# Optimization experiments

Measured on AMD Instinct MI355X. Metric: run time of the kernel, lower is better.

The kernel has to match this reference:

```python
import jax, jax.numpy as jnp
import numpy as np


def log_g(x):
    # log of g(x) = where(x>=0, x+0.5, sigmoid(x))
    return jnp.where(x >= 0, jnp.log(jax.nn.relu(x) + 0.5), -jax.nn.softplus(-x))


def heinsen_scan_log(log_coeffs, log_values):
    # associative scan in log space over seq dim (axis=1)
    a_star = jnp.cumsum(log_coeffs, axis=1)
    log_h0_plus_b_star = jax.lax.cumlogsumexp(log_values - a_star, axis=1)
    return jnp.exp(a_star + log_h0_plus_b_star)


def setup_inputs() -> dict:
    key = jax.random.key(0)
    k1, k2, k3 = jax.random.split(key, 3)
    B, S, D_IN, D_INNER, D_OUT = 4, 4096, 1024, 1024, 1024
    x = jax.random.normal(k1, (B, S, D_IN), dtype=jnp.float32)
    # xavier_normal for Linear(d_in, 2*d_inner): std = sqrt(2/(fan_in+fan_out))
    std_hg = float(np.sqrt(2.0 / (D_IN + 2 * D_INNER)))
    W_hg = jax.random.normal(k2, (2 * D_INNER, D_IN), dtype=jnp.float32) * std_hg
    std_out = float(np.sqrt(2.0 / (D_INNER + D_OUT)))
    W_out = jax.random.normal(k3, (D_OUT, D_INNER), dtype=jnp.float32) * std_out
    return {"x": x, "W_hg": W_hg, "W_out": W_out}


def reference(x, W_hg, W_out):
    # x: [B,S,Din]; W_hg: [2*Dinner, Din]; W_out: [Dout, Dinner]
    hg = jnp.einsum("bsd,ed->bse", x, W_hg)
    hidden, gate = jnp.split(hg, 2, axis=-1)
    log_coeffs = -jax.nn.softplus(gate)        # log(1 - z)
    log_z = -jax.nn.softplus(-gate)            # log(z)
    log_values = log_z + log_g(hidden)
    h = heinsen_scan_log(log_coeffs, log_values)  # [B,S,Dinner]
    out = jnp.einsum("bsd,od->bso", h, W_out)
    return out
```

## Files before the change

### kernel.cpp

```cpp
#include <hip/hip_runtime.h>
#include <math.h>


typedef unsigned short ushort_t;
typedef unsigned int uint_t;
typedef __attribute__((ext_vector_type(4))) float f32x4;
typedef __attribute__((ext_vector_type(8))) __bf16 bf16x8;
typedef __attribute__((ext_vector_type(8))) unsigned short u16x8;

constexpr int Bsz  = 4;
constexpr int S    = 4096;
constexpr int Din  = 1024;
constexpr int Dh   = 1024;
constexpr int M    = Bsz * S;
constexpr int NCH  = 64;
constexpr int CL   = S / NCH;

__device__ __forceinline__ unsigned short f2bf(float f) {
    unsigned int u = __float_as_uint(f);
    unsigned int r = (u + 0x7fffu + ((u >> 16) & 1u)) >> 16;
    return (unsigned short)r;
}
__device__ __forceinline__ float bf2f(unsigned short u) {
    return __uint_as_float(((unsigned int)u) << 16);
}
__device__ __forceinline__ float sigf(float x) {
    x = fminf(fmaxf(x, -30.f), 30.f);
    return 1.0f / (1.0f + __expf(-x));
}
__device__ __forceinline__ void gld_lds16(const ushort_t* g, ushort_t* l) {
    __builtin_amdgcn_global_load_lds(
        (const __attribute__((address_space(1))) void*)g,
        (__attribute__((address_space(3))) void*)l, 16, 0, 0);
}

__global__ __launch_bounds__(256) void cvt_all(
    const float* __restrict__ x, const float* __restrict__ whg,
    const float* __restrict__ wout,
    ushort_t* __restrict__ xb, ushort_t* __restrict__ whgb,
    ushort_t* __restrict__ woutb)
{
    constexpr int NX = M * Din / 8;
    constexpr int NW = 2048 * 1024 / 8;
    const int i = blockIdx.x * 256 + threadIdx.x;
    const float* src; ushort_t* dst; int k;
    if (i < NX)            { src = x;    dst = xb;    k = i; }
    else if (i < NX + NW)  { src = whg;  dst = whgb;  k = i - NX; }
    else                   { src = wout; dst = woutb; k = i - NX - NW; }
    const float4 a = ((const float4*)src)[(size_t)k * 2];
    const float4 b = ((const float4*)src)[(size_t)k * 2 + 1];
    u16x8 o;
    o[0] = f2bf(a.x); o[1] = f2bf(a.y); o[2] = f2bf(a.z); o[3] = f2bf(a.w);
    o[4] = f2bf(b.x); o[5] = f2bf(b.y); o[6] = f2bf(b.z); o[7] = f2bf(b.w);
    ((u16x8*)dst)[k] = o;
}

__global__ __launch_bounds__(512, 2) void gemm256(
    const ushort_t* __restrict__ A, int lda,
    const ushort_t* __restrict__ B, int ldb,
    ushort_t* __restrict__ Cout, int ldc, int K, int nbx_log2)
{
    __shared__ ushort_t lds[4][2][8192];

    const int P = K >> 5;

    const int nwg = gridDim.x;
    const int cpx = nwg >> 3;
    const int bid = blockIdx.x;
    const int swz = (bid & 7) * cpx + (bid >> 3);
    const int bx  = swz & ((1 << nbx_log2) - 1);
    const int by  = swz >> nbx_log2;
    const int bm0 = by * 256;
    const int bn0 = bx * 256;

    const int t  = threadIdx.x;
    const int w  = t >> 6;
    const int l  = t & 63;
    const int wr = w >> 2;
    const int wc = w & 3;

    const int fr = l & 15;
    const int kg = l >> 4;
    const int qp = kg ^ (((fr >> 3) & 1) << 1);
    const int a_base = wr * 4096 + fr * 32 + qp * 8;
    const int b_base = wc * 2048 + fr * 32 + qp * 8;

    const int rs = l >> 2;
    const int lq = (l & 3) ^ (((rs >> 3) & 1) << 1);
    const ushort_t* gA0 = A + (size_t)(bm0 + w * 16 + rs) * lda + lq * 8;
    const ushort_t* gA1 = gA0 + (size_t)128 * lda;
    const ushort_t* gB0 = B + (size_t)(bn0 + w * 16 + rs) * ldb + lq * 8;
    const ushort_t* gB1 = gB0 + (size_t)128 * ldb;

    f32x4 acc[8][4];
    #pragma unroll
    for (int i = 0; i < 8; ++i)
        #pragma unroll
        for (int j = 0; j < 4; ++j)
            acc[i][j] = (f32x4){0.f, 0.f, 0.f, 0.f};

    auto stage = [&](int p) {
        const int s2 = p & 3;
        const int ko = p * 32;
        gld_lds16(gA0 + ko, &lds[s2][0][w * 512]);
        gld_lds16(gA1 + ko, &lds[s2][0][w * 512 + 4096]);
        gld_lds16(gB0 + ko, &lds[s2][1][w * 512]);
        gld_lds16(gB1 + ko, &lds[s2][1][w * 512 + 4096]);
    };

    auto phase_body = [&](int p, bool do_stage) {
        __builtin_amdgcn_s_barrier();
        __builtin_amdgcn_sched_barrier(0);
        const int s = p & 3;
        const ushort_t* la = &lds[s][0][0];
        const ushort_t* lb = &lds[s][1][0];
        bf16x8 af[8], bfr[4];
        #pragma unroll
        for (int i = 0; i < 8; ++i)
            af[i] = *reinterpret_cast<const bf16x8*>(&la[a_base + i * 512]);
        #pragma unroll
        for (int j = 0; j < 4; ++j)
            bfr[j] = *reinterpret_cast<const bf16x8*>(&lb[b_base + j * 512]);
        if (do_stage) stage(p + 2);
        __builtin_amdgcn_sched_barrier(0);
        __builtin_amdgcn_s_setprio(1);
        #pragma unroll
        for (int i = 0; i < 8; ++i)
            #pragma unroll
            for (int j = 0; j < 4; ++j)
                acc[i][j] = __builtin_amdgcn_mfma_f32_16x16x32_bf16(
                    af[i], bfr[j], acc[i][j], 0, 0, 0);
        __builtin_amdgcn_s_setprio(0);
        __builtin_amdgcn_sched_barrier(0);
    };

    stage(0);
    stage(1);

    for (int p = 0; p < P - 1; ++p) {
        asm volatile("s_waitcnt vmcnt(4)" ::: "memory");
        phase_body(p, p < P - 2);
    }
    asm volatile("s_waitcnt vmcnt(0)" ::: "memory");
    phase_body(P - 1, false);

    #pragma unroll
    for (int i = 0; i < 8; ++i) {
        #pragma unroll
        for (int j = 0; j < 4; ++j) {
            const int col = bn0 + wc * 64 + j * 16 + fr;
            #pragma unroll
            for (int r = 0; r < 4; ++r) {
                const int row = bm0 + wr * 128 + i * 16 + kg * 4 + r;
                Cout[(size_t)row * ldc + col] = f2bf(acc[i][j][r]);
            }
        }
    }
}

__global__ __launch_bounds__(512, 4) void gemm128(
    const ushort_t* __restrict__ A, int lda,
    const ushort_t* __restrict__ B, int ldb,
    float* __restrict__ Cout, int ldc, int K, int nbx_log2)
{
    __shared__ ushort_t lds[3][12288];

    const int P = K >> 5;

    const int nwg = gridDim.x;
    const int cpx = nwg >> 3;
    const int bid = blockIdx.x;
    const int swz = (bid & 7) * cpx + (bid >> 3);
    const int bx  = swz & ((1 << nbx_log2) - 1);
    const int by  = swz >> nbx_log2;
    const int bm0 = by * 128;
    const int bn0 = bx * 256;

    const int t  = threadIdx.x;
    const int w  = t >> 6;
    const int l  = t & 63;
    const int wr = w >> 2;
    const int wc = w & 3;

    const int fr = l & 15;
    const int kg = l >> 4;
    const int qp = kg ^ (((fr >> 3) & 1) << 1);
    const int a_base = wr * 2048 + fr * 32 + qp * 8;
    const int b_base = 4096 + wc * 2048 + fr * 32 + qp * 8;

    const int rs = l >> 2;
    const int lq = (l & 3) ^ (((rs >> 3) & 1) << 1);
    const ushort_t* gA0 = A + (size_t)(bm0 + w * 16 + rs) * lda + lq * 8;
    const ushort_t* gB0 = B + (size_t)(bn0 + w * 16 + rs) * ldb + lq * 8;
    const ushort_t* gB1 = gB0 + (size_t)128 * ldb;

    f32x4 acc[4][4];
    #pragma unroll
    for (int i = 0; i < 4; ++i)
        #pragma unroll
        for (int j = 0; j < 4; ++j)
            acc[i][j] = (f32x4){0.f, 0.f, 0.f, 0.f};

    auto stage = [&](int p, int s) {
        ushort_t* base = &lds[s][0];
        const int ko = p * 32;
        gld_lds16(gA0 + ko, base + w * 512);
        gld_lds16(gB0 + ko, base + 4096 + w * 512);
        gld_lds16(gB1 + ko, base + 8192 + w * 512);
    };

    stage(0, 0);
    stage(1, 1);

    int scur = 0;
    int snxt2 = 2;
    #pragma unroll 1
    for (int p = 0; p < P; ++p) {
        if (p < P - 1)
            asm volatile("s_waitcnt vmcnt(3)" ::: "memory");
        else
            asm volatile("s_waitcnt vmcnt(0)" ::: "memory");
        __builtin_amdgcn_s_barrier();
        __builtin_amdgcn_sched_barrier(0);
        const ushort_t* ls = &lds[scur][0];
        bf16x8 af[4], bfr[4];
        #pragma unroll
        for (int i = 0; i < 4; ++i)
            af[i] = *reinterpret_cast<const bf16x8*>(&ls[a_base + i * 512]);
        #pragma unroll
        for (int j = 0; j < 4; ++j)
            bfr[j] = *reinterpret_cast<const bf16x8*>(&ls[b_base + j * 512]);
        if (p + 2 < P) stage(p + 2, snxt2);
        __builtin_amdgcn_sched_barrier(0);
        __builtin_amdgcn_s_setprio(1);
        #pragma unroll
        for (int i = 0; i < 4; ++i)
            #pragma unroll
            for (int j = 0; j < 4; ++j)
                acc[i][j] = __builtin_amdgcn_mfma_f32_16x16x32_bf16(
                    af[i], bfr[j], acc[i][j], 0, 0, 0);
        __builtin_amdgcn_s_setprio(0);
        __builtin_amdgcn_sched_barrier(0);
        scur  = (scur  == 2) ? 0 : scur + 1;
        snxt2 = (snxt2 == 2) ? 0 : snxt2 + 1;
    }

    #pragma unroll
    for (int i = 0; i < 4; ++i) {
        #pragma unroll
        for (int j = 0; j < 4; ++j) {
            const int col = bn0 + wc * 64 + j * 16 + fr;
            #pragma unroll
            for (int r = 0; r < 4; ++r) {
                const int row = bm0 + wr * 64 + i * 16 + kg * 4 + r;
                Cout[(size_t)row * ldc + col] = acc[i][j][r];
            }
        }
    }
}


__global__ __launch_bounds__(256) void scan_stage1(
    const ushort_t* __restrict__ hg, float* __restrict__ Abuf,
    float* __restrict__ hlbuf)
{
    const int bid   = blockIdx.x;
    const int half  = bid & 1;
    const int chunk = (bid >> 1) & (NCH - 1);
    const int b     = bid >> 7;
    const int t     = threadIdx.x;
    const int d     = half * 512 + 2 * t;
    const size_t rowbase = (size_t)(b * S + chunk * CL) * 2048 + d;

    float h0 = 0.f, h1 = 0.f, A0 = 1.f, A1 = 1.f;
    #pragma unroll 4
    for (int i = 0; i < CL; ++i) {
        const ushort_t* rp = hg + rowbase + (size_t)i * 2048;
        const uint_t hp = *(const uint_t*)rp;
        const uint_t gp = *(const uint_t*)(rp + 1024);
        const float hid0 = bf2f((ushort_t)hp), hid1 = bf2f((ushort_t)(hp >> 16));
        const float g0 = bf2f((ushort_t)gp),  g1 = bf2f((ushort_t)(gp >> 16));
        const float c0 = sigf(-g0), z0 = 1.f - c0;
        const float c1 = sigf(-g1), z1 = 1.f - c1;
        const float gv0 = (hid0 >= 0.f) ? (hid0 + 0.5f) : sigf(hid0);
        const float gv1 = (hid1 >= 0.f) ? (hid1 + 0.5f) : sigf(hid1);
        h0 = fmaf(c0, h0, z0 * gv0);  A0 *= c0;
        h1 = fmaf(c1, h1, z1 * gv1);  A1 *= c1;
    }
    const size_t pb = (size_t)(b * NCH + chunk) * 1024 + d;
    *(float2*)&Abuf[pb]  = make_float2(A0, A1);
    *(float2*)&hlbuf[pb] = make_float2(h0, h1);
}

__global__ __launch_bounds__(256) void scan_stage2(
    const float* __restrict__ Abuf, const float* __restrict__ hlbuf,
    float* __restrict__ Hs)
{
    const int g = blockIdx.x * 256 + threadIdx.x;
    const int d = g & (Dh - 1);
    const int b = g >> 10;
    float h = 0.0f;
    for (int ch = 0; ch < NCH; ++ch) {
        const size_t o = (size_t)(b * NCH + ch) * Dh + d;
        Hs[o] = h;
        h = fmaf(Abuf[o], h, hlbuf[o]);
    }
}

__global__ __launch_bounds__(256) void scan_stage3(
    const ushort_t* __restrict__ hg, const float* __restrict__ Hs,
    ushort_t* __restrict__ hout)
{
    const int bid   = blockIdx.x;
    const int half  = bid & 1;
    const int chunk = (bid >> 1) & (NCH - 1);
    const int b     = bid >> 7;
    const int t     = threadIdx.x;
    const int d     = half * 512 + 2 * t;
    const size_t rowbase = (size_t)(b * S + chunk * CL) * 2048 + d;
    const size_t hb      = (size_t)(b * S + chunk * CL) * 1024 + d;

    const float2 hs = *(const float2*)&Hs[(size_t)(b * NCH + chunk) * 1024 + d];
    float h0 = hs.x, h1 = hs.y;
    #pragma unroll 4
    for (int i = 0; i < CL; ++i) {
        const ushort_t* rp = hg + rowbase + (size_t)i * 2048;
        const uint_t hp = *(const uint_t*)rp;
        const uint_t gp = *(const uint_t*)(rp + 1024);
        const float hid0 = bf2f((ushort_t)hp), hid1 = bf2f((ushort_t)(hp >> 16));
        const float g0 = bf2f((ushort_t)gp),  g1 = bf2f((ushort_t)(gp >> 16));
        const float c0 = sigf(-g0), z0 = 1.f - c0;
        const float c1 = sigf(-g1), z1 = 1.f - c1;
        const float gv0 = (hid0 >= 0.f) ? (hid0 + 0.5f) : sigf(hid0);
        const float gv1 = (hid1 >= 0.f) ? (hid1 + 0.5f) : sigf(hid1);
        h0 = fmaf(c0, h0, z0 * gv0);
        h1 = fmaf(c1, h1, z1 * gv1);
        const uint_t o = (uint_t)f2bf(h0) | ((uint_t)f2bf(h1) << 16);
        *(uint_t*)(hout + hb + (size_t)i * 1024) = o;
    }
}

extern "C" void kernel_launch(void* const* d_in, const int* in_sizes, int n_in,
                              void* d_out, int out_size, void* d_ws, size_t ws_size,
                              hipStream_t stream)
{
    (void)in_sizes; (void)n_in; (void)out_size; (void)ws_size;
    const float* x    = (const float*)d_in[0];
    const float* Whg  = (const float*)d_in[1];
    const float* Wout = (const float*)d_in[2];
    float* out = (float*)d_out;

    ushort_t* hgbuf = (ushort_t*)d_ws;
    ushort_t* xb    = hgbuf + (size_t)M * 2048;
    ushort_t* whgb  = xb + (size_t)M * 1024;
    ushort_t* woutb = whgb + (size_t)2048 * 1024;
    float*    Abuf  = (float*)(woutb + (size_t)1024 * 1024);
    float*    hlbuf = Abuf + (size_t)Bsz * NCH * Dh;
    float*    Hsbuf = hlbuf + (size_t)Bsz * NCH * Dh;

    const dim3 blk(256);

    cvt_all<<<dim3(9728), blk, 0, stream>>>(x, Whg, Wout, xb, whgb, woutb);

    gemm256<<<dim3(512), dim3(512), 0, stream>>>(
        xb, Din, whgb, Din, hgbuf, 2048, Din, 3);

    scan_stage1<<<dim3(512), blk, 0, stream>>>(hgbuf, Abuf, hlbuf);
    scan_stage2<<<dim3(Bsz * Dh / 256), blk, 0, stream>>>(Abuf, hlbuf, Hsbuf);
    scan_stage3<<<dim3(512), blk, 0, stream>>>(hgbuf, Hsbuf, xb);

    gemm128<<<dim3(512), dim3(512), 0, stream>>>(
        xb, Dh, woutb, Din, out, 1024, Dh, 2);
}
```

Before: 207.7 us.

## Split GEMM K-step into two half-phases with staggered A/B staging; reuse for output GEMM

The 256x256 GEMM main loop now splits each K-step into two halves. Each half loads half of the A fragments and issues either the A or the B global-to-LDS prefetch, with extra barriers between halves. This interleaves LDS reads, global prefetch and MFMA work more finely, in the style of an 8-phase ping-pong schedule. The same templated kernel, with fp32 output, replaces the 128x256 output GEMM, which now runs on 256 blocks instead of 512. The cost is more barriers per step, and the output GEMM gets a larger tile with lower occupancy and fewer blocks than there are CUs.

Measured after the change: 209.8 us. Within noise of the previous version (+1.0%).

```diff
diff --git a/kernel.cpp b/kernel.cpp
--- a/kernel.cpp
+++ b/kernel.cpp
@@ -55,10 +55,11 @@
     ((u16x8*)dst)[k] = o;
 }
 
-__global__ __launch_bounds__(512, 2) void gemm256(
+template<bool OUT_BF16>
+__global__ __launch_bounds__(512, 2) void gemm8p(
     const ushort_t* __restrict__ A, int lda,
     const ushort_t* __restrict__ B, int ldb,
-    ushort_t* __restrict__ Cout, int ldc, int K, int nbx_log2)
+    void* __restrict__ Cout, int ldc, int K, int nbx_log2)
 {
     __shared__ ushort_t lds[4][2][8192];
 
@@ -99,50 +100,79 @@
         for (int j = 0; j < 4; ++j)
             acc[i][j] = (f32x4){0.f, 0.f, 0.f, 0.f};
 
-    auto stage = [&](int p) {
+    auto stageA = [&](int p) {
         const int s2 = p & 3;
         const int ko = p * 32;
         gld_lds16(gA0 + ko, &lds[s2][0][w * 512]);
         gld_lds16(gA1 + ko, &lds[s2][0][w * 512 + 4096]);
+    };
+    auto stageB = [&](int p) {
+        const int s2 = p & 3;
+        const int ko = p * 32;
         gld_lds16(gB0 + ko, &lds[s2][1][w * 512]);
         gld_lds16(gB1 + ko, &lds[s2][1][w * 512 + 4096]);
     };
 
-    auto phase_body = [&](int p, bool do_stage) {
-        __builtin_amdgcn_s_barrier();
-        __builtin_amdgcn_sched_barrier(0);
+    stageA(0); stageB(0); stageA(1); stageB(1);
+    asm volatile("s_waitcnt vmcnt(4)" ::: "memory");
+    __builtin_amdgcn_s_barrier();
+    __builtin_amdgcn_sched_barrier(0);
+
+    #pragma unroll 1
+    for (int p = 0; p < P; ++p) {
         const int s = p & 3;
         const ushort_t* la = &lds[s][0][0];
         const ushort_t* lb = &lds[s][1][0];
-        bf16x8 af[8], bfr[4];
-        #pragma unroll
-        for (int i = 0; i < 8; ++i)
-            af[i] = *reinterpret_cast<const bf16x8*>(&la[a_base + i * 512]);
+        bf16x8 bfr[4], af0[4], af1[4];
+
         #pragma unroll
         for (int j = 0; j < 4; ++j)
             bfr[j] = *reinterpret_cast<const bf16x8*>(&lb[b_base + j * 512]);
-        if (do_stage) stage(p + 2);
+        #pragma unroll
+        for (int i = 0; i < 4; ++i)
+            af0[i] = *reinterpret_cast<const bf16x8*>(&la[a_base + i * 512]);
+        if (p + 2 < P) stageA(p + 2);
+        __builtin_amdgcn_sched_barrier(0);
+        __builtin_amdgcn_s_barrier();
+        asm volatile("s_waitcnt lgkmcnt(0)" ::: "memory");
         __builtin_amdgcn_sched_barrier(0);
         __builtin_amdgcn_s_setprio(1);
         #pragma unroll
-        for (int i = 0; i < 8; ++i)
+        for (int i = 0; i < 4; ++i)
             #pragma unroll
             for (int j = 0; j < 4; ++j)
                 acc[i][j] = __builtin_amdgcn_mfma_f32_16x16x32_bf16(
-                    af[i], bfr[j], acc[i][j], 0, 0, 0);
+                    af0[i], bfr[j], acc[i][j], 0, 0, 0);
         __builtin_amdgcn_s_setprio(0);
         __builtin_amdgcn_sched_barrier(0);
-    };
-
-    stage(0);
-    stage(1);
-
-    for (int p = 0; p < P - 1; ++p) {
-        asm volatile("s_waitcnt vmcnt(4)" ::: "memory");
-        phase_body(p, p < P - 2);
-    }
-    asm volatile("s_waitcnt vmcnt(0)" ::: "memory");
-    phase_body(P - 1, false);
+        #pragma unroll
+        for (int i = 0; i < 4; ++i)
+            af1[i] = *reinterpret_cast<const bf16x8*>(&la[a_base + (4 + i) * 512]);
+        __builtin_amdgcn_sched_barrier(0);
+        __builtin_amdgcn_s_barrier();
+        __builtin_amdgcn_sched_barrier(0);
+
+        if (p + 2 < P) stageB(p + 2);
+        __builtin_amdgcn_sched_barrier(0);
+        if (p + 2 < P)
+            asm volatile("s_waitcnt vmcnt(4)" ::: "memory");
+        else if (p + 1 < P)
+            asm volatile("s_waitcnt vmcnt(0)" ::: "memory");
+        __builtin_amdgcn_s_barrier();
+        asm volatile("s_waitcnt lgkmcnt(0)" ::: "memory");
+        __builtin_amdgcn_sched_barrier(0);
+        __builtin_amdgcn_s_setprio(1);
+        #pragma unroll
+        for (int i = 0; i < 4; ++i)
+            #pragma unroll
+            for (int j = 0; j < 4; ++j)
+                acc[4 + i][j] = __builtin_amdgcn_mfma_f32_16x16x32_bf16(
+                    af1[i], bfr[j], acc[4 + i][j], 0, 0, 0);
+        __builtin_amdgcn_s_setprio(0);
+        __builtin_amdgcn_sched_barrier(0);
+        __builtin_amdgcn_s_barrier();
+        __builtin_amdgcn_sched_barrier(0);
+    }
 
     #pragma unroll
     for (int i = 0; i < 8; ++i) {
@@ -152,108 +182,10 @@
             #pragma unroll
             for (int r = 0; r < 4; ++r) {
                 const int row = bm0 + wr * 128 + i * 16 + kg * 4 + r;
-                Cout[(size_t)row * ldc + col] = f2bf(acc[i][j][r]);
-            }
-        }
-    }
-}
-
-__global__ __launch_bounds__(512, 4) void gemm128(
-    const ushort_t* __restrict__ A, int lda,
-    const ushort_t* __restrict__ B, int ldb,
-    float* __restrict__ Cout, int ldc, int K, int nbx_log2)
-{
-    __shared__ ushort_t lds[3][12288];
-
-    const int P = K >> 5;
-
-    const int nwg = gridDim.x;
-    const int cpx = nwg >> 3;
-    const int bid = blockIdx.x;
-    const int swz = (bid & 7) * cpx + (bid >> 3);
-    const int bx  = swz & ((1 << nbx_log2) - 1);
-    const int by  = swz >> nbx_log2;
-    const int bm0 = by * 128;
-    const int bn0 = bx * 256;
-
-    const int t  = threadIdx.x;
-    const int w  = t >> 6;
-    const int l  = t & 63;
-    const int wr = w >> 2;
-    const int wc = w & 3;
-
-    const int fr = l & 15;
-    const int kg = l >> 4;
-    const int qp = kg ^ (((fr >> 3) & 1) << 1);
-    const int a_base = wr * 2048 + fr * 32 + qp * 8;
-    const int b_base = 4096 + wc * 2048 + fr * 32 + qp * 8;
-
-    const int rs = l >> 2;
-    const int lq = (l & 3) ^ (((rs >> 3) & 1) << 1);
-    const ushort_t* gA0 = A + (size_t)(bm0 + w * 16 + rs) * lda + lq * 8;
-    const ushort_t* gB0 = B + (size_t)(bn0 + w * 16 + rs) * ldb + lq * 8;
-    const ushort_t* gB1 = gB0 + (size_t)128 * ldb;
-
-    f32x4 acc[4][4];
-    #pragma unroll
-    for (int i = 0; i < 4; ++i)
-        #pragma unroll
-        for (int j = 0; j < 4; ++j)
-            acc[i][j] = (f32x4){0.f, 0.f, 0.f, 0.f};
-
-    auto stage = [&](int p, int s) {
-        ushort_t* base = &lds[s][0];
-        const int ko = p * 32;
-        gld_lds16(gA0 + ko, base + w * 512);
-        gld_lds16(gB0 + ko, base + 4096 + w * 512);
-        gld_lds16(gB1 + ko, base + 8192 + w * 512);
-    };
-
-    stage(0, 0);
-    stage(1, 1);
-
-    int scur = 0;
-    int snxt2 = 2;
-    #pragma unroll 1
-    for (int p = 0; p < P; ++p) {
-        if (p < P - 1)
-            asm volatile("s_waitcnt vmcnt(3)" ::: "memory");
-        else
-            asm volatile("s_waitcnt vmcnt(0)" ::: "memory");
-        __builtin_amdgcn_s_barrier();
-        __builtin_amdgcn_sched_barrier(0);
-        const ushort_t* ls = &lds[scur][0];
-        bf16x8 af[4], bfr[4];
-        #pragma unroll
-        for (int i = 0; i < 4; ++i)
-            af[i] = *reinterpret_cast<const bf16x8*>(&ls[a_base + i * 512]);
-        #pragma unroll
-        for (int j = 0; j < 4; ++j)
-            bfr[j] = *reinterpret_cast<const bf16x8*>(&ls[b_base + j * 512]);
-        if (p + 2 < P) stage(p + 2, snxt2);
-        __builtin_amdgcn_sched_barrier(0);
-        __builtin_amdgcn_s_setprio(1);
-        #pragma unroll
-        for (int i = 0; i < 4; ++i)
-            #pragma unroll
-            for (int j = 0; j < 4; ++j)
-                acc[i][j] = __builtin_amdgcn_mfma_f32_16x16x32_bf16(
-                    af[i], bfr[j], acc[i][j], 0, 0, 0);
-        __builtin_amdgcn_s_setprio(0);
-        __builtin_amdgcn_sched_barrier(0);
-        scur  = (scur  == 2) ? 0 : scur + 1;
-        snxt2 = (snxt2 == 2) ? 0 : snxt2 + 1;
-    }
-
-    #pragma unroll
-    for (int i = 0; i < 4; ++i) {
-        #pragma unroll
-        for (int j = 0; j < 4; ++j) {
-            const int col = bn0 + wc * 64 + j * 16 + fr;
-            #pragma unroll
-            for (int r = 0; r < 4; ++r) {
-                const int row = bm0 + wr * 64 + i * 16 + kg * 4 + r;
-                Cout[(size_t)row * ldc + col] = acc[i][j][r];
+                if (OUT_BF16)
+                    ((ushort_t*)Cout)[(size_t)row * ldc + col] = f2bf(acc[i][j][r]);
+                else
+                    ((float*)Cout)[(size_t)row * ldc + col] = acc[i][j][r];
             }
         }
     }
@@ -362,13 +294,13 @@
 
     cvt_all<<<dim3(9728), blk, 0, stream>>>(x, Whg, Wout, xb, whgb, woutb);
 
-    gemm256<<<dim3(512), dim3(512), 0, stream>>>(
+    gemm8p<true><<<dim3(512), dim3(512), 0, stream>>>(
         xb, Din, whgb, Din, hgbuf, 2048, Din, 3);
 
     scan_stage1<<<dim3(512), blk, 0, stream>>>(hgbuf, Abuf, hlbuf);
     scan_stage2<<<dim3(Bsz * Dh / 256), blk, 0, stream>>>(Abuf, hlbuf, Hsbuf);
     scan_stage3<<<dim3(512), blk, 0, stream>>>(hgbuf, Hsbuf, xb);
 
-    gemm128<<<dim3(512), dim3(512), 0, stream>>>(
+    gemm8p<false><<<dim3(256), dim3(512), 0, stream>>>(
         xb, Dh, woutb, Din, out, 1024, Dh, 2);
 }
```

## Rework output GEMM to 4 waves with 128x64 per-wave tiles

Applied to the files above, without the earlier changes.

The output-projection GEMM kernel goes from 8 waves (2x4 layout, 64x64 per wave) to 4 waves, each computing a 128x64 sub-tile of the same 128x256 block. Each wave now loads 8 A fragments and 4 B fragments per k-step and issues 32 MFMAs, which raises MFMA work per LDS read. Each thread also issues 6 global-to-LDS loads per stage, with the vmcnt wait adjusted and the last iteration peeled. The cost is more accumulator registers and fewer waves per block for hiding latency.

Result: no change. 207.7 us (median of 3 runs) (+0.0%).

```diff
diff --git a/kernel.cpp b/kernel.cpp
--- a/kernel.cpp
+++ b/kernel.cpp
@@ -158,7 +158,7 @@
     }
 }
 
-__global__ __launch_bounds__(512, 4) void gemm128(
+__global__ __launch_bounds__(256) void gemm2w4(
     const ushort_t* __restrict__ A, int lda,
     const ushort_t* __restrict__ B, int ldb,
     float* __restrict__ Cout, int ldc, int K, int nbx_log2)
@@ -176,27 +176,28 @@
     const int bm0 = by * 128;
     const int bn0 = bx * 256;
 
-    const int t  = threadIdx.x;
-    const int w  = t >> 6;
-    const int l  = t & 63;
-    const int wr = w >> 2;
-    const int wc = w & 3;
+    const int t = threadIdx.x;
+    const int w = t >> 6;
+    const int l = t & 63;
 
     const int fr = l & 15;
     const int kg = l >> 4;
     const int qp = kg ^ (((fr >> 3) & 1) << 1);
-    const int a_base = wr * 2048 + fr * 32 + qp * 8;
-    const int b_base = 4096 + wc * 2048 + fr * 32 + qp * 8;
+    const int a_base = fr * 32 + qp * 8;
+    const int b_base = 4096 + w * 2048 + fr * 32 + qp * 8;
 
     const int rs = l >> 2;
     const int lq = (l & 3) ^ (((rs >> 3) & 1) << 1);
-    const ushort_t* gA0 = A + (size_t)(bm0 + w * 16 + rs) * lda + lq * 8;
-    const ushort_t* gB0 = B + (size_t)(bn0 + w * 16 + rs) * ldb + lq * 8;
-    const ushort_t* gB1 = gB0 + (size_t)128 * ldb;
-
-    f32x4 acc[4][4];
+    const ushort_t* gA0 = A + (size_t)(bm0 + w * 32 + rs) * lda + lq * 8;
+    const ushort_t* gA1 = gA0 + (size_t)16 * lda;
+    const ushort_t* gB0 = B + (size_t)(bn0 + w * 64 + rs) * ldb + lq * 8;
+    const ushort_t* gB1 = gB0 + (size_t)16 * ldb;
+    const ushort_t* gB2 = gB0 + (size_t)32 * ldb;
+    const ushort_t* gB3 = gB0 + (size_t)48 * ldb;
+
+    f32x4 acc[8][4];
     #pragma unroll
-    for (int i = 0; i < 4; ++i)
+    for (int i = 0; i < 8; ++i)
         #pragma unroll
         for (int j = 0; j < 4; ++j)
             acc[i][j] = (f32x4){0.f, 0.f, 0.f, 0.f};
@@ -204,55 +205,60 @@
     auto stage = [&](int p, int s) {
         ushort_t* base = &lds[s][0];
         const int ko = p * 32;
-        gld_lds16(gA0 + ko, base + w * 512);
-        gld_lds16(gB0 + ko, base + 4096 + w * 512);
-        gld_lds16(gB1 + ko, base + 8192 + w * 512);
+        gld_lds16(gA0 + ko, base + w * 1024);
+        gld_lds16(gA1 + ko, base + w * 1024 + 512);
+        gld_lds16(gB0 + ko, base + 4096 + w * 2048);
+        gld_lds16(gB1 + ko, base + 4096 + w * 2048 + 512);
+        gld_lds16(gB2 + ko, base + 4096 + w * 2048 + 1024);
+        gld_lds16(gB3 + ko, base + 4096 + w * 2048 + 1536);
     };
 
-    stage(0, 0);
-    stage(1, 1);
-
-    int scur = 0;
-    int snxt2 = 2;
-    #pragma unroll 1
-    for (int p = 0; p < P; ++p) {
-        if (p < P - 1)
-            asm volatile("s_waitcnt vmcnt(3)" ::: "memory");
-        else
-            asm volatile("s_waitcnt vmcnt(0)" ::: "memory");
+    auto phase_body = [&](int p, int s, int s2, bool do_stage) {
         __builtin_amdgcn_s_barrier();
         __builtin_amdgcn_sched_barrier(0);
-        const ushort_t* ls = &lds[scur][0];
-        bf16x8 af[4], bfr[4];
-        #pragma unroll
-        for (int i = 0; i < 4; ++i)
+        const ushort_t* ls = &lds[s][0];
+        bf16x8 af[8], bfr[4];
+        #pragma unroll
+        for (int i = 0; i < 8; ++i)
             af[i] = *reinterpret_cast<const bf16x8*>(&ls[a_base + i * 512]);
         #pragma unroll
         for (int j = 0; j < 4; ++j)
             bfr[j] = *reinterpret_cast<const bf16x8*>(&ls[b_base + j * 512]);
-        if (p + 2 < P) stage(p + 2, snxt2);
+        if (do_stage) stage(p + 2, s2);
         __builtin_amdgcn_sched_barrier(0);
         __builtin_amdgcn_s_setprio(1);
         #pragma unroll
-        for (int i = 0; i < 4; ++i)
+        for (int i = 0; i < 8; ++i)
             #pragma unroll
             for (int j = 0; j < 4; ++j)
                 acc[i][j] = __builtin_amdgcn_mfma_f32_16x16x32_bf16(
                     af[i], bfr[j], acc[i][j], 0, 0, 0);
         __builtin_amdgcn_s_setprio(0);
         __builtin_amdgcn_sched_barrier(0);
-        scur  = (scur  == 2) ? 0 : scur + 1;
-        snxt2 = (snxt2 == 2) ? 0 : snxt2 + 1;
-    }
+    };
+
+    stage(0, 0);
+    stage(1, 1);
+
+    int scur = 0, snx2 = 2;
+    #pragma unroll 1
+    for (int p = 0; p < P - 1; ++p) {
+        asm volatile("s_waitcnt vmcnt(6)" ::: "memory");
+        phase_body(p, scur, snx2, p < P - 2);
+        scur = (scur == 2) ? 0 : scur + 1;
+        snx2 = (snx2 == 2) ? 0 : snx2 + 1;
+    }
+    asm volatile("s_waitcnt vmcnt(0)" ::: "memory");
+    phase_body(P - 1, scur, snx2, false);
 
     #pragma unroll
-    for (int i = 0; i < 4; ++i) {
+    for (int i = 0; i < 8; ++i) {
         #pragma unroll
         for (int j = 0; j < 4; ++j) {
-            const int col = bn0 + wc * 64 + j * 16 + fr;
+            const int col = bn0 + w * 64 + j * 16 + fr;
             #pragma unroll
             for (int r = 0; r < 4; ++r) {
-                const int row = bm0 + wr * 64 + i * 16 + kg * 4 + r;
+                const int row = bm0 + i * 16 + kg * 4 + r;
                 Cout[(size_t)row * ldc + col] = acc[i][j][r];
             }
         }
@@ -369,6 +375,6 @@
     scan_stage2<<<dim3(Bsz * Dh / 256), blk, 0, stream>>>(Abuf, hlbuf, Hsbuf);
     scan_stage3<<<dim3(512), blk, 0, stream>>>(hgbuf, Hsbuf, xb);
 
-    gemm128<<<dim3(512), dim3(512), 0, stream>>>(
+    gemm2w4<<<dim3(512), blk, 0, stream>>>(
         xb, Dh, woutb, Din, out, 1024, Dh, 2);
 }
```

## Fuse x fp32-to-bf16 conversion into first GEMM by loading fp32 tiles to LDS

Applied to the files above, without the earlier changes.

The separate conversion pass over x (16M floats) is removed. The first GEMM now streams fp32 x tiles straight into LDS and converts them to bf16 in registers before the MFMAs. This drops one full read of x and one write plus re-read of the bf16 copy. In exchange, the A tile costs twice the LDS bytes and global traffic per stage, the pipeline shrinks from 4 to 3 LDS slots of 48KB, and conversion ALU work is added to the inner loop. That larger LDS footprint may limit occupancy.

Measured after the change: 208.5 us. No clear change (+0.4%).

```diff
diff --git a/kernel.cpp b/kernel.cpp
--- a/kernel.cpp
+++ b/kernel.cpp
@@ -28,25 +28,21 @@
     x = fminf(fmaxf(x, -30.f), 30.f);
     return 1.0f / (1.0f + __expf(-x));
 }
-__device__ __forceinline__ void gld_lds16(const ushort_t* g, ushort_t* l) {
+__device__ __forceinline__ void gld_lds16(const void* g, void* l) {
     __builtin_amdgcn_global_load_lds(
         (const __attribute__((address_space(1))) void*)g,
         (__attribute__((address_space(3))) void*)l, 16, 0, 0);
 }
 
-__global__ __launch_bounds__(256) void cvt_all(
-    const float* __restrict__ x, const float* __restrict__ whg,
-    const float* __restrict__ wout,
-    ushort_t* __restrict__ xb, ushort_t* __restrict__ whgb,
-    ushort_t* __restrict__ woutb)
-{
-    constexpr int NX = M * Din / 8;
+__global__ __launch_bounds__(256) void cvt_w(
+    const float* __restrict__ whg, const float* __restrict__ wout,
+    ushort_t* __restrict__ whgb, ushort_t* __restrict__ woutb)
+{
     constexpr int NW = 2048 * 1024 / 8;
     const int i = blockIdx.x * 256 + threadIdx.x;
     const float* src; ushort_t* dst; int k;
-    if (i < NX)            { src = x;    dst = xb;    k = i; }
-    else if (i < NX + NW)  { src = whg;  dst = whgb;  k = i - NX; }
-    else                   { src = wout; dst = woutb; k = i - NX - NW; }
+    if (i < NW) { src = whg;  dst = whgb;  k = i; }
+    else        { src = wout; dst = woutb; k = i - NW; }
     const float4 a = ((const float4*)src)[(size_t)k * 2];
     const float4 b = ((const float4*)src)[(size_t)k * 2 + 1];
     u16x8 o;
@@ -55,13 +51,14 @@
     ((u16x8*)dst)[k] = o;
 }
 
-__global__ __launch_bounds__(512, 2) void gemm256(
-    const ushort_t* __restrict__ A, int lda,
+__global__ __launch_bounds__(512, 2) void gemm1_xf32(
+    const float* __restrict__ X,
     const ushort_t* __restrict__ B, int ldb,
-    ushort_t* __restrict__ Cout, int ldc, int K, int nbx_log2)
-{
-    __shared__ ushort_t lds[4][2][8192];
-
+    ushort_t* __restrict__ Cout, int ldc, int nbx_log2)
+{
+    constexpr int K = Din;
+    constexpr int SLOT = 49152;
+    __shared__ char lds[3][SLOT];
     const int P = K >> 5;
 
     const int nwg = gridDim.x;
@@ -81,14 +78,14 @@
 
     const int fr = l & 15;
     const int kg = l >> 4;
+    const int a_fbase = (wr * 128 + fr) * 32 + (((kg * 2) ^ (fr & 7)) * 4);
     const int qp = kg ^ (((fr >> 3) & 1) << 1);
-    const int a_base = wr * 4096 + fr * 32 + qp * 8;
-    const int b_base = wc * 2048 + fr * 32 + qp * 8;
-
+    const int b_byte = 32768 + wc * 4096 + fr * 64 + qp * 16;
+
+    const float* gA = X + (size_t)(bm0 + w * 32 + (l >> 3)) * Din
+                        + ((l & 7) ^ (l >> 3)) * 4;
     const int rs = l >> 2;
     const int lq = (l & 3) ^ (((rs >> 3) & 1) << 1);
-    const ushort_t* gA0 = A + (size_t)(bm0 + w * 16 + rs) * lda + lq * 8;
-    const ushort_t* gA1 = gA0 + (size_t)128 * lda;
     const ushort_t* gB0 = B + (size_t)(bn0 + w * 16 + rs) * ldb + lq * 8;
     const ushort_t* gB1 = gB0 + (size_t)128 * ldb;
 
@@ -99,29 +96,49 @@
         for (int j = 0; j < 4; ++j)
             acc[i][j] = (f32x4){0.f, 0.f, 0.f, 0.f};
 
-    auto stage = [&](int p) {
-        const int s2 = p & 3;
-        const int ko = p * 32;
-        gld_lds16(gA0 + ko, &lds[s2][0][w * 512]);
-        gld_lds16(gA1 + ko, &lds[s2][0][w * 512 + 4096]);
-        gld_lds16(gB0 + ko, &lds[s2][1][w * 512]);
-        gld_lds16(gB1 + ko, &lds[s2][1][w * 512 + 4096]);
+    auto stage = [&](int p, int s) {
+        char* base = &lds[s][0];
+        const int koA = p * 32;
+        #pragma unroll
+        for (int q = 0; q < 4; ++q)
+            gld_lds16(gA + (size_t)q * 8 * Din + koA,
+                      base + w * 4096 + q * 1024 + l * 16);
+        const int koB = p * 32;
+        gld_lds16(gB0 + koB, base + 32768 + w * 1024);
+        gld_lds16(gB1 + koB, base + 32768 + w * 1024 + 8192);
     };
 
-    auto phase_body = [&](int p, bool do_stage) {
+    stage(0, 0);
+    stage(1, 1);
+
+    int scur = 0, snx2 = 2;
+    #pragma unroll 1
+    for (int p = 0; p < P; ++p) {
+        if (p < P - 1)
+            asm volatile("s_waitcnt vmcnt(6)" ::: "memory");
+        else
+            asm volatile("s_waitcnt vmcnt(0)" ::: "memory");
         __builtin_amdgcn_s_barrier();
         __builtin_amdgcn_sched_barrier(0);
-        const int s = p & 3;
-        const ushort_t* la = &lds[s][0][0];
-        const ushort_t* lb = &lds[s][1][0];
+        const float*    fA = (const float*)&lds[scur][0];
+        const ushort_t* lB = (const ushort_t*)&lds[scur][0];
         bf16x8 af[8], bfr[4];
         #pragma unroll
-        for (int i = 0; i < 8; ++i)
-            af[i] = *reinterpret_cast<const bf16x8*>(&la[a_base + i * 512]);
+        for (int i = 0; i < 8; ++i) {
+            const int lo = a_fbase + i * 512;
+            const f32x4 va = *(const f32x4*)&fA[lo];
+            const f32x4 vb = *(const f32x4*)&fA[lo ^ 4];
+            union { bf16x8 v; __bf16 e[8]; } u;
+            u.e[0] = (__bf16)va[0]; u.e[1] = (__bf16)va[1];
+            u.e[2] = (__bf16)va[2]; u.e[3] = (__bf16)va[3];
+            u.e[4] = (__bf16)vb[0]; u.e[5] = (__bf16)vb[1];
+            u.e[6] = (__bf16)vb[2]; u.e[7] = (__bf16)vb[3];
+            af[i] = u.v;
+        }
         #pragma unroll
         for (int j = 0; j < 4; ++j)
-            bfr[j] = *reinterpret_cast<const bf16x8*>(&lb[b_base + j * 512]);
-        if (do_stage) stage(p + 2);
+            bfr[j] = *(const bf16x8*)((const char*)lB + b_byte + j * 1024);
+        if (p + 2 < P) stage(p + 2, snx2);
         __builtin_amdgcn_sched_barrier(0);
         __builtin_amdgcn_s_setprio(1);
         #pragma unroll
@@ -132,17 +149,9 @@
                     af[i], bfr[j], acc[i][j], 0, 0, 0);
         __builtin_amdgcn_s_setprio(0);
         __builtin_amdgcn_sched_barrier(0);
-    };
-
-    stage(0);
-    stage(1);
-
-    for (int p = 0; p < P - 1; ++p) {
-        asm volatile("s_waitcnt vmcnt(4)" ::: "memory");
-        phase_body(p, p < P - 2);
-    }
-    asm volatile("s_waitcnt vmcnt(0)" ::: "memory");
-    phase_body(P - 1, false);
+        scur = (scur == 2) ? 0 : scur + 1;
+        snx2 = (snx2 == 2) ? 0 : snx2 + 1;
+    }
 
     #pragma unroll
     for (int i = 0; i < 8; ++i) {
@@ -212,8 +221,7 @@
     stage(0, 0);
     stage(1, 1);
 
-    int scur = 0;
-    int snxt2 = 2;
+    int scur = 0, snxt2 = 2;
     #pragma unroll 1
     for (int p = 0; p < P; ++p) {
         if (p < P - 1)
@@ -351,8 +359,8 @@
     float* out = (float*)d_out;
 
     ushort_t* hgbuf = (ushort_t*)d_ws;
-    ushort_t* xb    = hgbuf + (size_t)M * 2048;
-    ushort_t* whgb  = xb + (size_t)M * 1024;
+    ushort_t* hb    = hgbuf + (size_t)M * 2048;
+    ushort_t* whgb  = hb + (size_t)M * 1024;
     ushort_t* woutb = whgb + (size_t)2048 * 1024;
     float*    Abuf  = (float*)(woutb + (size_t)1024 * 1024);
     float*    hlbuf = Abuf + (size_t)Bsz * NCH * Dh;
@@ -360,15 +368,15 @@
 
     const dim3 blk(256);
 
-    cvt_all<<<dim3(9728), blk, 0, stream>>>(x, Whg, Wout, xb, whgb, woutb);
-
-    gemm256<<<dim3(512), dim3(512), 0, stream>>>(
-        xb, Din, whgb, Din, hgbuf, 2048, Din, 3);
+    cvt_w<<<dim3(1536), blk, 0, stream>>>(Whg, Wout, whgb, woutb);
+
+    gemm1_xf32<<<dim3(512), dim3(512), 0, stream>>>(
+        x, whgb, Din, hgbuf, 2048, 3);
 
     scan_stage1<<<dim3(512), blk, 0, stream>>>(hgbuf, Abuf, hlbuf);
     scan_stage2<<<dim3(Bsz * Dh / 256), blk, 0, stream>>>(Abuf, hlbuf, Hsbuf);
-    scan_stage3<<<dim3(512), blk, 0, stream>>>(hgbuf, Hsbuf, xb);
+    scan_stage3<<<dim3(512), blk, 0, stream>>>(hgbuf, Hsbuf, hb);
 
     gemm128<<<dim3(512), dim3(512), 0, stream>>>(
-        xb, Dh, woutb, Din, out, 1024, Dh, 2);
-}
+        hb, Dh, woutb, Din, out, 1024, Dh, 2);
+}
```
